# Kernel optimization log

Measured on AMD Instinct MI355X. Metric: run time of the kernel, lower is better.

## Reference

```python
import jax, jax.numpy as jnp
import numpy as np

B, T, D_IN, D_HID, TAG = 32, 2048, 1024, 2048, 2

def setup_inputs() -> dict:
    key = jax.random.key(0)
    k1, k2, k3, k4, k5, k6 = jax.random.split(key, 6)
    h = jax.random.normal(k1, (B, T, D_IN), dtype=jnp.float32)
    # valid lengths in [1, T] (avoid zero-length divide)
    text_len = jnp.maximum(jax.random.randint(k2, (B,), 0, T), 1)
    s1 = 1.0 / np.sqrt(D_IN)
    s2 = 1.0 / np.sqrt(D_HID)
    W1 = jax.random.uniform(k3, (D_HID, D_IN), minval=-s1, maxval=s1, dtype=jnp.float32)
    b1 = jax.random.uniform(k4, (D_HID,), minval=-s1, maxval=s1, dtype=jnp.float32)
    W2 = jax.random.uniform(k5, (TAG, D_HID), minval=-s2, maxval=s2, dtype=jnp.float32)
    b2 = jax.random.uniform(k6, (TAG,), minval=-s2, maxval=s2, dtype=jnp.float32)
    return {"h": h, "text_len": text_len, "W1": W1, "b1": b1, "W2": W2, "b2": b2}

def reference(h, text_len, W1, b1, W2, b2):
    # lin1 + relu (dropout is identity at inference)
    hidden = jax.nn.relu(jnp.einsum('btd,hd->bth', h, W1) + b1)  # [B,T,H]
    # masked mean over the first text_len[i] positions per sample
    mask = (jnp.arange(hidden.shape[1])[None, :] < text_len[:, None]).astype(hidden.dtype)  # [B,T]
    pooled = jnp.einsum('bth,bt->bh', hidden, mask) / text_len[:, None].astype(hidden.dtype)  # [B,H]
    score = jnp.einsum('bh,th->bt', pooled, W2) + b2  # [B,TAG]
    return score
```

## Files before the change

kernel.cpp:

```cpp
#include <hip/hip_runtime.h>
#include <hip/hip_bf16.h>

#define B_   32
#define T_   2048
#define DIN  1024
#define DHID 2048
#define BM   128
#define BN   128
#define BK   64

typedef __attribute__((ext_vector_type(8))) short bf16x8;
typedef __attribute__((ext_vector_type(4))) float f32x4;
typedef __attribute__((ext_vector_type(4))) int   i32x4;

union BF8 { bf16x8 v; i32x4 i; unsigned int u[4]; };

__device__ inline unsigned int f2bf_u(float f) {
    unsigned int u = __float_as_uint(f);
    return (u + 0x7FFFu + ((u >> 16) & 1u)) >> 16;
}
__device__ inline unsigned int pack2bf(float a, float b) {
    return f2bf_u(a) | (f2bf_u(b) << 16);
}

__global__ void convert_w1(const float* __restrict__ W1,
                           unsigned short* __restrict__ W1b,
                           float* __restrict__ pooled) {
    int idx = blockIdx.x * blockDim.x + threadIdx.x;
    float4 f = ((const float4*)W1)[idx];
    ((uint2*)W1b)[idx] = uint2{pack2bf(f.x, f.y), pack2bf(f.z, f.w)};
    if (idx < B_ * DHID / 4) ((float4*)pooled)[idx] = float4{0.f, 0.f, 0.f, 0.f};
}

__global__ void convert_h(const float* __restrict__ h,
                          const int*   __restrict__ text_len,
                          unsigned short* __restrict__ hb) {
    const int b   = blockIdx.y;
    const int idx = blockIdx.x * 256 + threadIdx.x;
    const int t   = idx >> 7;
    const size_t gi = (size_t)b * (T_ * DIN / 8) + idx;
    uint4 o;
    if (t < text_len[b]) {
        float4 f0 = ((const float4*)h)[gi * 2];
        float4 f1 = ((const float4*)h)[gi * 2 + 1];
        o.x = pack2bf(f0.x, f0.y);
        o.y = pack2bf(f0.z, f0.w);
        o.z = pack2bf(f1.x, f1.y);
        o.w = pack2bf(f1.z, f1.w);
    } else {
        o = uint4{0u, 0u, 0u, 0u};
    }
    ((uint4*)hb)[gi] = o;
}

__global__ __launch_bounds__(256) void scorer_gemm_lds(
    const unsigned short* __restrict__ hb,
    const int*            __restrict__ text_len,
    const unsigned short* __restrict__ W1b,
    const float*          __restrict__ b1,
    float*                __restrict__ pooled) {

    const int nt  = blockIdx.x;
    const int tt  = blockIdx.y;
    const int b   = blockIdx.z;
    const int len = text_len[b];
    const int t0  = tt * BM;
    if (t0 >= len) return;
    const int n0  = nt * BN;

    __shared__ unsigned short lds[(BM + BN) * BK];
    unsigned short* As = lds;
    unsigned short* Bs = lds + BM * BK;

    const int tid  = threadIdx.x;
    const int lane = tid & 63;
    const int wid  = tid >> 6;
    const int wr   = wid >> 1;
    const int wc   = wid & 1;
    const int quad = lane >> 4;
    const int l15  = lane & 15;
    const int sw   = l15 & 7;

    const int srow = lane >> 3;
    const int schunk = (lane & 7) ^ ((lane >> 3) & 7);
    const int skc  = schunk * 8;

    f32x4 acc[4][4] = {};
    const size_t abase = ((size_t)b * T_ + t0) * DIN;

    for (int kt = 0; kt < DIN / BK; ++kt) {
        const int k0 = kt * BK;
#pragma unroll
        for (int j = 0; j < 4; ++j) {
            int s = wid * 4 + j;
            int row = s * 8 + srow;
            const unsigned short* gp = hb + abase + (size_t)row * DIN + k0 + skc;
            __builtin_amdgcn_global_load_lds(
                (const __attribute__((address_space(1))) void*)gp,
                (__attribute__((address_space(3))) void*)(As + s * 512),
                16, 0, 0);
        }
#pragma unroll
        for (int j = 0; j < 4; ++j) {
            int s = wid * 4 + j;
            int row = s * 8 + srow;
            const unsigned short* gp = W1b + (size_t)(n0 + row) * DIN + k0 + skc;
            __builtin_amdgcn_global_load_lds(
                (const __attribute__((address_space(1))) void*)gp,
                (__attribute__((address_space(3))) void*)(Bs + s * 512),
                16, 0, 0);
        }
        __syncthreads();

#pragma unroll
        for (int kk = 0; kk < 2; ++kk) {
            BF8 a[4], w[4];
            const int chunk = (kk * 4 + quad) ^ sw;
#pragma unroll
            for (int mi = 0; mi < 4; ++mi)
                a[mi].i = *(const i32x4*)(As + (wr * 64 + mi * 16 + l15) * BK + chunk * 8);
#pragma unroll
            for (int ni = 0; ni < 4; ++ni)
                w[ni].i = *(const i32x4*)(Bs + (wc * 64 + ni * 16 + l15) * BK + chunk * 8);
#pragma unroll
            for (int mi = 0; mi < 4; ++mi)
#pragma unroll
                for (int ni = 0; ni < 4; ++ni)
                    acc[mi][ni] = __builtin_amdgcn_mfma_f32_16x16x32_bf16(
                        a[mi].v, w[ni].v, acc[mi][ni], 0, 0, 0);
        }
        __syncthreads();
    }

#pragma unroll
    for (int ni = 0; ni < 4; ++ni) {
        int n = n0 + wc * 64 + ni * 16 + l15;
        float bias = b1[n];
        float colsum = 0.f;
#pragma unroll
        for (int mi = 0; mi < 4; ++mi) {
            int trow = t0 + wr * 64 + mi * 16 + quad * 4;
#pragma unroll
            for (int r = 0; r < 4; ++r) {
                float v = acc[mi][ni][r] + bias;
                v = v > 0.f ? v : 0.f;
                if (trow + r < len) colsum += v;
            }
        }
        colsum += __shfl_xor(colsum, 16);
        colsum += __shfl_xor(colsum, 32);
        if (quad == 0) atomicAdd(&pooled[b * DHID + n], colsum);
    }
}

__global__ void scorer_gemm_direct(const float* __restrict__ hin,
                                   const int*   __restrict__ text_len,
                                   const unsigned short* __restrict__ W1b,
                                   const float* __restrict__ b1,
                                   float*       __restrict__ pooled) {
    const int tt  = blockIdx.x;
    const int b   = blockIdx.y;
    const int len = text_len[b];
    const int t0  = tt * 64;
    if (t0 >= len) return;
    const int tid = threadIdx.x, lane = tid & 63, wid = tid >> 6;
    const int wrow = wid >> 1, wcol = wid & 1, quad = lane >> 4, l15 = lane & 15;
    const float* aptr[2];
#pragma unroll
    for (int mi = 0; mi < 2; ++mi)
        aptr[mi] = hin + ((size_t)b * T_ + t0 + wrow * 32 + mi * 16 + l15) * DIN + quad * 8;
    for (int nout = 0; nout < DHID / 128; ++nout) {
        const int nbase = nout * 128;
        f32x4 acc[2][4] = {};
        const unsigned short* bptr[4];
        float b1v[4];
#pragma unroll
        for (int ni = 0; ni < 4; ++ni) {
            int n = nbase + wcol * 64 + ni * 16 + l15;
            bptr[ni] = W1b + (size_t)n * DIN + quad * 8;
            b1v[ni]  = b1[n];
        }
        for (int k = 0; k < DIN; k += 32) {
            BF8 a[2], w[4];
#pragma unroll
            for (int mi = 0; mi < 2; ++mi) {
                float4 f0 = *(const float4*)(aptr[mi] + k);
                float4 f1 = *(const float4*)(aptr[mi] + k + 4);
                a[mi].u[0] = pack2bf(f0.x, f0.y);
                a[mi].u[1] = pack2bf(f0.z, f0.w);
                a[mi].u[2] = pack2bf(f1.x, f1.y);
                a[mi].u[3] = pack2bf(f1.z, f1.w);
            }
#pragma unroll
            for (int ni = 0; ni < 4; ++ni) w[ni].i = *(const i32x4*)(bptr[ni] + k);
#pragma unroll
            for (int mi = 0; mi < 2; ++mi)
#pragma unroll
                for (int ni = 0; ni < 4; ++ni)
                    acc[mi][ni] = __builtin_amdgcn_mfma_f32_16x16x32_bf16(
                        a[mi].v, w[ni].v, acc[mi][ni], 0, 0, 0);
        }
#pragma unroll
        for (int ni = 0; ni < 4; ++ni) {
            float colsum = 0.f;
#pragma unroll
            for (int mi = 0; mi < 2; ++mi) {
                int trow = t0 + wrow * 32 + mi * 16 + quad * 4;
#pragma unroll
                for (int r = 0; r < 4; ++r) {
                    float v = acc[mi][ni][r] + b1v[ni];
                    v = v > 0.f ? v : 0.f;
                    if (trow + r < len) colsum += v;
                }
            }
            colsum += __shfl_xor(colsum, 16);
            colsum += __shfl_xor(colsum, 32);
            if (quad == 0)
                atomicAdd(&pooled[b * DHID + nbase + wcol * 64 + ni * 16 + l15], colsum);
        }
    }
}

__global__ void finalize_k(const float* __restrict__ pooled,
                           const int*   __restrict__ text_len,
                           const float* __restrict__ W2,
                           const float* __restrict__ b2,
                           float*       __restrict__ out) {
    int b = blockIdx.x, tid = threadIdx.x;
    float s0 = 0.f, s1 = 0.f;
    for (int hh = tid; hh < DHID; hh += 256) {
        float p = pooled[b * DHID + hh];
        s0 += p * W2[hh];
        s1 += p * W2[DHID + hh];
    }
#pragma unroll
    for (int off = 32; off > 0; off >>= 1) {
        s0 += __shfl_down(s0, off);
        s1 += __shfl_down(s1, off);
    }
    __shared__ float r0[4], r1[4];
    int wid = tid >> 6, lane = tid & 63;
    if (lane == 0) { r0[wid] = s0; r1[wid] = s1; }
    __syncthreads();
    if (tid == 0) {
        float inv = 1.0f / (float)text_len[b];
        out[b * 2 + 0] = (r0[0] + r0[1] + r0[2] + r0[3]) * inv + b2[0];
        out[b * 2 + 1] = (r1[0] + r1[1] + r1[2] + r1[3]) * inv + b2[1];
    }
}

extern "C" void kernel_launch(void* const* d_in, const int* in_sizes, int n_in,
                              void* d_out, int out_size, void* d_ws, size_t ws_size,
                              hipStream_t stream) {
    const float* hin      = (const float*)d_in[0];
    const int*   text_len = (const int*)  d_in[1];
    const float* W1       = (const float*)d_in[2];
    const float* b1       = (const float*)d_in[3];
    const float* W2       = (const float*)d_in[4];
    const float* b2       = (const float*)d_in[5];
    float* out = (float*)d_out;

    const size_t HB_BYTES  = (size_t)B_ * T_ * DIN * 2;
    const size_t W1B_BYTES = (size_t)DHID * DIN * 2;
    const size_t NEED      = HB_BYTES + W1B_BYTES + (size_t)B_ * DHID * 4;

    if (ws_size >= NEED) {
        unsigned short* hb     = (unsigned short*)d_ws;
        unsigned short* W1b    = (unsigned short*)((char*)d_ws + HB_BYTES);
        float*          pooled = (float*)((char*)d_ws + HB_BYTES + W1B_BYTES);

        convert_w1<<<(DHID * DIN / 4) / 256, 256, 0, stream>>>(W1, W1b, pooled);
        dim3 hgrid((T_ * DIN / 8) / 256, B_);
        convert_h<<<hgrid, 256, 0, stream>>>(hin, text_len, hb);

        dim3 grid(DHID / BN, T_ / BM, B_);
        scorer_gemm_lds<<<grid, 256, 0, stream>>>(hb, text_len, W1b, b1, pooled);
        finalize_k<<<B_, 256, 0, stream>>>(pooled, text_len, W2, b2, out);
    } else {
        unsigned short* W1b    = (unsigned short*)d_ws;
        float*          pooled = (float*)((char*)d_ws + W1B_BYTES);
        (void)hipMemsetAsync(pooled, 0, B_ * DHID * sizeof(float), stream);
        convert_w1<<<(DHID * DIN / 4) / 256, 256, 0, stream>>>(W1, W1b, pooled);
        dim3 grid(T_ / 64, B_);
        scorer_gemm_direct<<<grid, 256, 0, stream>>>(hin, text_len, W1b, b1, pooled);
        finalize_k<<<B_, 256, 0, stream>>>(pooled, text_len, W2, b2, out);
    }
}
```

Baseline: 568.4 us.

## Restructure GEMM into 256x256 double-buffered 8-wave ping-pong pipeline

Replaces the 128x128 single-buffered LDS GEMM with a 256x256 tile, 512-thread kernel that double-buffers A and B in LDS. Each K step is split into four MFMA phases interleaved with staged global-to-LDS loads, explicit barriers, vmcnt waits and setprio, so loads overlap compute and operand reuse per tile goes up. The h conversion now skips writing rows beyond text_len, which saves store bandwidth but leaves those bf16 rows uninitialized. Those rows are still read by partial tiles and masked out in the epilogue. The larger tile means more wasted work on the last partial tile of each sequence and higher register and LDS pressure.

```diff
diff --git a/kernel.cpp b/kernel.cpp
--- a/kernel.cpp
+++ b/kernel.cpp
@@ -5,9 +5,12 @@
 #define T_   2048
 #define DIN  1024
 #define DHID 2048
-#define BM   128
-#define BN   128
+#define TAG  2
+
+#define BM   256
+#define BN   256
 #define BK   64
+#define NT   (DIN / BK)
 
 typedef __attribute__((ext_vector_type(8))) short bf16x8;
 typedef __attribute__((ext_vector_type(4))) float f32x4;
@@ -22,6 +25,10 @@
 __device__ inline unsigned int pack2bf(float a, float b) {
     return f2bf_u(a) | (f2bf_u(b) << 16);
 }
+
+#define BARRIER()  asm volatile("s_barrier" ::: "memory")
+#define LGKM0()    asm volatile("s_waitcnt lgkmcnt(0)" ::: "memory")
+#define VMCNT(n)   asm volatile("s_waitcnt vmcnt(" #n ")" ::: "memory")
 
 __global__ void convert_w1(const float* __restrict__ W1,
                            unsigned short* __restrict__ W1b,
@@ -38,22 +45,19 @@
     const int b   = blockIdx.y;
     const int idx = blockIdx.x * 256 + threadIdx.x;
     const int t   = idx >> 7;
+    if (t >= text_len[b]) return;
     const size_t gi = (size_t)b * (T_ * DIN / 8) + idx;
+    float4 f0 = ((const float4*)h)[gi * 2];
+    float4 f1 = ((const float4*)h)[gi * 2 + 1];
     uint4 o;
-    if (t < text_len[b]) {
-        float4 f0 = ((const float4*)h)[gi * 2];
-        float4 f1 = ((const float4*)h)[gi * 2 + 1];
-        o.x = pack2bf(f0.x, f0.y);
-        o.y = pack2bf(f0.z, f0.w);
-        o.z = pack2bf(f1.x, f1.y);
-        o.w = pack2bf(f1.z, f1.w);
-    } else {
-        o = uint4{0u, 0u, 0u, 0u};
-    }
+    o.x = pack2bf(f0.x, f0.y);
+    o.y = pack2bf(f0.z, f0.w);
+    o.z = pack2bf(f1.x, f1.y);
+    o.w = pack2bf(f1.z, f1.w);
     ((uint4*)hb)[gi] = o;
 }
 
-__global__ __launch_bounds__(256) void scorer_gemm_lds(
+__global__ __launch_bounds__(512, 2) void scorer_gemm_8ph(
     const unsigned short* __restrict__ hb,
     const int*            __restrict__ text_len,
     const unsigned short* __restrict__ W1b,
@@ -68,78 +72,157 @@
     if (t0 >= len) return;
     const int n0  = nt * BN;
 
-    __shared__ unsigned short lds[(BM + BN) * BK];
-    unsigned short* As = lds;
-    unsigned short* Bs = lds + BM * BK;
+    __shared__ __align__(16) unsigned short lds[4 * BM * BK];
 
     const int tid  = threadIdx.x;
     const int lane = tid & 63;
     const int wid  = tid >> 6;
-    const int wr   = wid >> 1;
-    const int wc   = wid & 1;
+    const int wm   = wid >> 2;
+    const int wn   = wid & 3;
     const int quad = lane >> 4;
     const int l15  = lane & 15;
-    const int sw   = l15 & 7;
-
-    const int srow = lane >> 3;
-    const int schunk = (lane & 7) ^ ((lane >> 3) & 7);
-    const int skc  = schunk * 8;
-
-    f32x4 acc[4][4] = {};
-    const size_t abase = ((size_t)b * T_ + t0) * DIN;
-
-    for (int kt = 0; kt < DIN / BK; ++kt) {
-        const int k0 = kt * BK;
-#pragma unroll
-        for (int j = 0; j < 4; ++j) {
-            int s = wid * 4 + j;
-            int row = s * 8 + srow;
-            const unsigned short* gp = hb + abase + (size_t)row * DIN + k0 + skc;
+
+    const int srow   = lane >> 3;
+    const int schunk = (lane & 7) ^ srow;
+    const unsigned short* gA = hb  + ((size_t)b * T_ + t0 + wid * 8 + srow) * DIN + schunk * 8;
+    const unsigned short* gB = W1b + ((size_t)(n0 + wid * 8 + srow)) * DIN + schunk * 8;
+    const int sdst = wid * 512;
+
+    auto stageA = [&](int d, int h, int k0) {
+#pragma unroll
+        for (int i = 0; i < 2; ++i) {
+            const unsigned short* gp = gA + (size_t)(h * 128 + i * 64) * DIN + k0;
             __builtin_amdgcn_global_load_lds(
                 (const __attribute__((address_space(1))) void*)gp,
-                (__attribute__((address_space(3))) void*)(As + s * 512),
+                (__attribute__((address_space(3))) void*)(lds + d * 16384 + (h * 128 + i * 64) * 64 + sdst),
                 16, 0, 0);
         }
-#pragma unroll
-        for (int j = 0; j < 4; ++j) {
-            int s = wid * 4 + j;
-            int row = s * 8 + srow;
-            const unsigned short* gp = W1b + (size_t)(n0 + row) * DIN + k0 + skc;
+    };
+    auto stageB = [&](int d, int h, int k0) {
+#pragma unroll
+        for (int i = 0; i < 2; ++i) {
+            const unsigned short* gp = gB + (size_t)(h * 128 + i * 64) * DIN + k0;
             __builtin_amdgcn_global_load_lds(
                 (const __attribute__((address_space(1))) void*)gp,
-                (__attribute__((address_space(3))) void*)(Bs + s * 512),
+                (__attribute__((address_space(3))) void*)(lds + 32768 + d * 16384 + (h * 128 + i * 64) * 64 + sdst),
                 16, 0, 0);
         }
-        __syncthreads();
-
-#pragma unroll
-        for (int kk = 0; kk < 2; ++kk) {
-            BF8 a[4], w[4];
-            const int chunk = (kk * 4 + quad) ^ sw;
-#pragma unroll
-            for (int mi = 0; mi < 4; ++mi)
-                a[mi].i = *(const i32x4*)(As + (wr * 64 + mi * 16 + l15) * BK + chunk * 8);
-#pragma unroll
-            for (int ni = 0; ni < 4; ++ni)
-                w[ni].i = *(const i32x4*)(Bs + (wc * 64 + ni * 16 + l15) * BK + chunk * 8);
-#pragma unroll
-            for (int mi = 0; mi < 4; ++mi)
-#pragma unroll
-                for (int ni = 0; ni < 4; ++ni)
+    };
+
+    auto rdA = [&](const unsigned short* As, int mi, int ks) -> i32x4 {
+        int row  = (mi >> 2) * 128 + wm * 64 + (mi & 3) * 16 + l15;
+        int slot = (ks * 4 + quad) ^ (l15 & 7);
+        return *(const i32x4*)(As + row * 64 + slot * 8);
+    };
+    auto rdB = [&](const unsigned short* Bs, int ni, int ks) -> i32x4 {
+        int row  = (ni >> 1) * 128 + wn * 32 + (ni & 1) * 16 + l15;
+        int slot = (ks * 4 + quad) ^ (l15 & 7);
+        return *(const i32x4*)(Bs + row * 64 + slot * 8);
+    };
+
+    f32x4 acc[8][4] = {};
+    BF8 a[4][2], bb[4][2];
+
+    stageA(0, 0, 0);  stageB(0, 0, 0);  stageB(0, 1, 0);  stageA(0, 1, 0);
+    stageA(1, 0, BK); stageB(1, 0, BK); stageB(1, 1, BK);
+    VMCNT(6);
+    BARRIER();
+
+    for (int t = 0; t < NT; ++t) {
+        const int k0 = t * BK;
+        const unsigned short* As = lds + (t & 1) * 16384;
+        const unsigned short* Bs = lds + 32768 + (t & 1) * 16384;
+
+#pragma unroll
+        for (int mi = 0; mi < 4; ++mi)
+#pragma unroll
+            for (int ks = 0; ks < 2; ++ks)
+                a[mi][ks].i = rdA(As, mi, ks);
+#pragma unroll
+        for (int ni = 0; ni < 2; ++ni)
+#pragma unroll
+            for (int ks = 0; ks < 2; ++ks)
+                bb[ni][ks].i = rdB(Bs, ni, ks);
+        if (t + 1 < NT) stageA((t + 1) & 1, 1, k0 + BK);
+        BARRIER();
+        LGKM0();
+        __builtin_amdgcn_s_setprio(1);
+#pragma unroll
+        for (int mi = 0; mi < 4; ++mi)
+#pragma unroll
+            for (int ni = 0; ni < 2; ++ni)
+#pragma unroll
+                for (int ks = 0; ks < 2; ++ks)
                     acc[mi][ni] = __builtin_amdgcn_mfma_f32_16x16x32_bf16(
-                        a[mi].v, w[ni].v, acc[mi][ni], 0, 0, 0);
-        }
-        __syncthreads();
+                        a[mi][ks].v, bb[ni][ks].v, acc[mi][ni], 0, 0, 0);
+        __builtin_amdgcn_s_setprio(0);
+        BARRIER();
+
+#pragma unroll
+        for (int ni = 2; ni < 4; ++ni)
+#pragma unroll
+            for (int ks = 0; ks < 2; ++ks)
+                bb[ni][ks].i = rdB(Bs, ni, ks);
+        if (t + 2 < NT) stageA(t & 1, 0, k0 + 2 * BK);
+        BARRIER();
+        LGKM0();
+        __builtin_amdgcn_s_setprio(1);
+#pragma unroll
+        for (int mi = 0; mi < 4; ++mi)
+#pragma unroll
+            for (int ni = 2; ni < 4; ++ni)
+#pragma unroll
+                for (int ks = 0; ks < 2; ++ks)
+                    acc[mi][ni] = __builtin_amdgcn_mfma_f32_16x16x32_bf16(
+                        a[mi][ks].v, bb[ni][ks].v, acc[mi][ni], 0, 0, 0);
+        __builtin_amdgcn_s_setprio(0);
+        BARRIER();
+
+#pragma unroll
+        for (int mi = 0; mi < 4; ++mi)
+#pragma unroll
+            for (int ks = 0; ks < 2; ++ks)
+                a[mi][ks].i = rdA(As, mi + 4, ks);
+        if (t + 2 < NT) stageB(t & 1, 0, k0 + 2 * BK);
+        BARRIER();
+        LGKM0();
+        __builtin_amdgcn_s_setprio(1);
+#pragma unroll
+        for (int mi = 0; mi < 4; ++mi)
+#pragma unroll
+            for (int ni = 2; ni < 4; ++ni)
+#pragma unroll
+                for (int ks = 0; ks < 2; ++ks)
+                    acc[4 + mi][ni] = __builtin_amdgcn_mfma_f32_16x16x32_bf16(
+                        a[mi][ks].v, bb[ni][ks].v, acc[4 + mi][ni], 0, 0, 0);
+        __builtin_amdgcn_s_setprio(0);
+        BARRIER();
+
+        if (t + 2 < NT) stageB(t & 1, 1, k0 + 2 * BK);
+        if (t < NT - 2)       { VMCNT(6); }
+        else if (t == NT - 2) { VMCNT(0); }
+        BARRIER();
+        __builtin_amdgcn_s_setprio(1);
+#pragma unroll
+        for (int mi = 0; mi < 4; ++mi)
+#pragma unroll
+            for (int ni = 0; ni < 2; ++ni)
+#pragma unroll
+                for (int ks = 0; ks < 2; ++ks)
+                    acc[4 + mi][ni] = __builtin_amdgcn_mfma_f32_16x16x32_bf16(
+                        a[mi][ks].v, bb[ni][ks].v, acc[4 + mi][ni], 0, 0, 0);
+        __builtin_amdgcn_s_setprio(0);
+        BARRIER();
     }
 
 #pragma unroll
     for (int ni = 0; ni < 4; ++ni) {
-        int n = n0 + wc * 64 + ni * 16 + l15;
+        int n = n0 + (ni >> 1) * 128 + wn * 32 + (ni & 1) * 16 + l15;
         float bias = b1[n];
         float colsum = 0.f;
 #pragma unroll
-        for (int mi = 0; mi < 4; ++mi) {
-            int trow = t0 + wr * 64 + mi * 16 + quad * 4;
+        for (int mi = 0; mi < 8; ++mi) {
+            int trow = t0 + (mi >> 2) * 128 + wm * 64 + (mi & 3) * 16 + quad * 4;
 #pragma unroll
             for (int r = 0; r < 4; ++r) {
                 float v = acc[mi][ni][r] + bias;
@@ -274,7 +357,7 @@
         convert_h<<<hgrid, 256, 0, stream>>>(hin, text_len, hb);
 
         dim3 grid(DHID / BN, T_ / BM, B_);
-        scorer_gemm_lds<<<grid, 256, 0, stream>>>(hb, text_len, W1b, b1, pooled);
+        scorer_gemm_8ph<<<grid, 512, 0, stream>>>(hb, text_len, W1b, b1, pooled);
         finalize_k<<<B_, 256, 0, stream>>>(pooled, text_len, W2, b2, out);
     } else {
         unsigned short* W1b    = (unsigned short*)d_ws;
```

Result: faster. 535.9 us (-5.7%).
